# Optimization experiments

Measured on AMD Instinct MI355X. Metric: run time of the kernel, lower is better.

## Reference

```python
import jax, jax.numpy as jnp
import numpy as np

MARGIN = 0.5

def setup_inputs() -> dict:
    key = jax.random.key(0)
    k1, k2 = jax.random.split(key)
    inputs = jax.random.normal(k1, (8192, 256), dtype=jnp.float32)
    target = jax.random.randint(k2, (8192,), 0, 100, dtype=jnp.int64)
    return {"inputs": inputs, "target": target}

def reference(inputs, target):
    N = inputs.shape[0]
    # pairwise squared distances via ||xi||^2 + ||xj||^2 - 2 xi.xj
    sq = jnp.sum(inputs * inputs, axis=1)  # [N]
    gram = inputs @ inputs.T               # [N, N]
    distance = sq[:, None] + sq[None, :] - 2.0 * gram  # [N, N]
    R = (target[None, :] == target[:, None]).astype(inputs.dtype)  # [N, N]
    loss = R * distance + (1.0 - R) * jnp.maximum(MARGIN - distance, 0.0)
    return jnp.sum(loss) / (N * (N - 1.0) * 2.0)
```

## Files before the change

kernel.cpp:

```cpp
#include <hip/hip_runtime.h>
#include <stdint.h>

#define N      8192
#define KDIM   256
#define BM     128
#define TILES  (N / BM)
#define NPAIRS (TILES * (TILES + 1) / 2)
#define MARGIN 0.5f
#define SCALE1 0x7f7f7f7f

typedef float f32x4 __attribute__((ext_vector_type(4)));
typedef int   i32x4 __attribute__((ext_vector_type(4)));
typedef int   i32x8 __attribute__((ext_vector_type(8)));

__device__ __forceinline__ void async_copy16(const void* g, void* l) {
    __builtin_amdgcn_global_load_lds(
        (__attribute__((address_space(1))) void*)(g),
        (__attribute__((address_space(3))) void*)(l),
        16, 0, 0);
}

#if !__has_builtin(__builtin_amdgcn_cvt_pk_fp8_f32)
__device__ __forceinline__ uint32_t f2e4m3(float f) {
    uint32_t u = __float_as_uint(f);
    uint32_t s = (u >> 24) & 0x80u;
    uint32_t au = u & 0x7fffffffu;
    if (au == 0) return s;
    int32_t  exp = (int32_t)(au >> 23) - 127;
    uint32_t man = (au & 0x7fffffu) | 0x800000u;
    uint32_t code;
    if (exp >= -6) {
        code = (uint32_t)((exp + 7) << 3) | ((man >> 20) & 7u);
        uint32_t rem = man & 0xFFFFFu;
        if (rem > 0x80000u || (rem == 0x80000u && (code & 1u))) code++;
    } else {
        int shift = 14 - exp;
        if (shift > 24) return s;
        code = man >> shift;
        uint32_t rem = man & ((1u << shift) - 1u);
        uint32_t h = 1u << (shift - 1);
        if (rem > h || (rem == h && (code & 1u))) code++;
    }
    return s | code;
}
__device__ __forceinline__ uint32_t pack_fp8x4(float4 v) {
    return f2e4m3(v.x) | (f2e4m3(v.y) << 8) | (f2e4m3(v.z) << 16) |
           (f2e4m3(v.w) << 24);
}
#else
__device__ __forceinline__ uint32_t pack_fp8x4(float4 v) {
    int pk = __builtin_amdgcn_cvt_pk_fp8_f32(v.x, v.y, 0, false);
    pk = __builtin_amdgcn_cvt_pk_fp8_f32(v.z, v.w, pk, true);
    return (uint32_t)pk;
}
#endif

__global__ __launch_bounds__(256) void prep_kernel(
        const float* __restrict__ X, uint8_t* __restrict__ Xq,
        float* __restrict__ sq) {
    int row  = blockIdx.x * 4 + (threadIdx.x >> 6);
    int lane = threadIdx.x & 63;

    float4 v = *((const float4*)(X + (size_t)row * KDIM) + lane);
    float ss = v.x * v.x + v.y * v.y + v.z * v.z + v.w * v.w;
    uint32_t pk = pack_fp8x4(v);

    int h   = lane >> 5;
    int g   = (lane >> 2) & 7;
    int pos = g ^ (row & 7);
    *(uint32_t*)(Xq + (size_t)row * 256 + h * 128 + pos * 16 + (lane & 3) * 4) = pk;

    #pragma unroll
    for (int o = 32; o > 0; o >>= 1) ss += __shfl_down(ss, o, 64);
    if (lane == 0) sq[row] = ss;
}

__global__ __launch_bounds__(256, 4) void loss_kernel(
        const uint8_t* __restrict__ Xq, const float* __restrict__ sq,
        const int* __restrict__ tgt, float* __restrict__ partials) {
    const int p = blockIdx.x;
    float tf = 2.0f * TILES + 1.0f;
    int bi = (int)((tf - sqrtf(tf * tf - 8.0f * (float)p)) * 0.5f);
    if (bi < 0) bi = 0;
    while (bi > 0 && (bi * TILES - bi * (bi - 1) / 2) > p) --bi;
    while (((bi + 1) * TILES - (bi + 1) * bi / 2) <= p) ++bi;
    const int bj = bi + (p - (bi * TILES - bi * (bi - 1) / 2));

    __shared__ __align__(16) uint8_t As[BM * 128];
    __shared__ __align__(16) uint8_t Bs[BM * 128];
    __shared__ float sqa_s[BM], sqb_s[BM];
    __shared__ int   ta_s[BM],  tb_s[BM];
    __shared__ float wsum[4];

    const int tid  = threadIdx.x;
    const int wave = tid >> 6;
    const int lane = tid & 63;

    if (tid < 128) {
        sqa_s[tid] = sq[bi * BM + tid];
        ta_s[tid]  = tgt[bi * BM + tid];
    } else {
        int r = tid - 128;
        sqb_s[r] = sq[bj * BM + r];
        tb_s[r]  = tgt[bj * BM + r];
    }

    const int lrow = lane >> 3;
    const int lb   = (lane & 7) * 16;
    const uint8_t* gA = Xq + ((size_t)bi * BM + wave * 32 + lrow) * 256 + lb;
    const uint8_t* gB = Xq + ((size_t)bj * BM + wave * 32 + lrow) * 256 + lb;
    uint8_t* lA = As + wave * 32 * 128;
    uint8_t* lB = Bs + wave * 32 * 128;

    const int frow  = lane & 15;
    const int fquad = lane >> 4;
    const int wm = (wave >> 1) * 64;
    const int wn = (wave & 1) * 64;
    const int key  = frow & 7;
    const int off0 = ((fquad * 2 + 0) ^ key) * 16;
    const int off1 = ((fquad * 2 + 1) ^ key) * 16;
    const uint8_t* aBp = As + (wm + frow) * 128;
    const uint8_t* bBp = Bs + (wn + frow) * 128;

    f32x4 acc[4][4];
    #pragma unroll
    for (int im = 0; im < 4; ++im)
        #pragma unroll
        for (int in = 0; in < 4; ++in)
            acc[im][in] = (f32x4){0.f, 0.f, 0.f, 0.f};

    #pragma unroll
    for (int h = 0; h < 2; ++h) {
        #pragma unroll
        for (int q = 0; q < 4; ++q) {
            async_copy16(gA + h * 128 + q * 8 * 256, lA + q * 1024);
            async_copy16(gB + h * 128 + q * 8 * 256, lB + q * 1024);
        }
        __syncthreads();

        i32x8 a8[4];
        #pragma unroll
        for (int im = 0; im < 4; ++im) {
            i32x4 al = *(const i32x4*)(aBp + im * 16 * 128 + off0);
            i32x4 ah = *(const i32x4*)(aBp + im * 16 * 128 + off1);
            a8[im] = __builtin_shufflevector(al, ah, 0, 1, 2, 3, 4, 5, 6, 7);
        }
        #pragma unroll
        for (int in = 0; in < 4; ++in) {
            i32x4 bl = *(const i32x4*)(bBp + in * 16 * 128 + off0);
            i32x4 bh = *(const i32x4*)(bBp + in * 16 * 128 + off1);
            i32x8 b8 = __builtin_shufflevector(bl, bh, 0, 1, 2, 3, 4, 5, 6, 7);
            #pragma unroll
            for (int im = 0; im < 4; ++im)
                acc[im][in] = __builtin_amdgcn_mfma_scale_f32_16x16x128_f8f6f4(
                    a8[im], b8, acc[im][in], 0, 0,
                    0, SCALE1, 0, SCALE1);
        }
        if (h == 0) __syncthreads();
    }

    float lsum = 0.0f;
    if (bi != bj) {
        #pragma unroll
        for (int im = 0; im < 4; ++im) {
            #pragma unroll
            for (int in = 0; in < 4; ++in) {
                #pragma unroll
                for (int r = 0; r < 4; ++r) {
                    int rl = wm + im * 16 + fquad * 4 + r;
                    int cl = wn + in * 16 + frow;
                    float d = fmaf(-2.0f, acc[im][in][r],
                                   sqa_s[rl] + sqb_s[cl]);
                    lsum += (ta_s[rl] == tb_s[cl]) ? d
                                                   : fmaxf(MARGIN - d, 0.0f);
                }
            }
        }
        lsum *= 2.0f;
    } else {
        #pragma unroll
        for (int im = 0; im < 4; ++im) {
            #pragma unroll
            for (int in = 0; in < 4; ++in) {
                #pragma unroll
                for (int r = 0; r < 4; ++r) {
                    int rl = wm + im * 16 + fquad * 4 + r;
                    int cl = wn + in * 16 + frow;
                    float d = fmaf(-2.0f, acc[im][in][r],
                                   sqa_s[rl] + sqb_s[cl]);
                    float c = (ta_s[rl] == tb_s[cl]) ? d
                                                     : fmaxf(MARGIN - d, 0.0f);
                    float w = (rl < cl) ? 2.0f : ((rl == cl) ? 1.0f : 0.0f);
                    lsum += w * c;
                }
            }
        }
    }

    #pragma unroll
    for (int o = 32; o > 0; o >>= 1) lsum += __shfl_down(lsum, o, 64);
    if (lane == 0) wsum[wave] = lsum;
    __syncthreads();
    if (tid == 0) partials[p] = wsum[0] + wsum[1] + wsum[2] + wsum[3];
}

__global__ __launch_bounds__(256) void reduce_kernel(
        const float* __restrict__ partials, float* __restrict__ out,
        int n, float scale) {
    float s = 0.0f;
    for (int i = threadIdx.x; i < n; i += 256) s += partials[i];
    __shared__ float w[4];
    #pragma unroll
    for (int o = 32; o > 0; o >>= 1) s += __shfl_down(s, o, 64);
    int wave = threadIdx.x >> 6, lane = threadIdx.x & 63;
    if (lane == 0) w[wave] = s;
    __syncthreads();
    if (threadIdx.x == 0) out[0] = (w[0] + w[1] + w[2] + w[3]) * scale;
}

extern "C" void kernel_launch(void* const* d_in, const int* in_sizes, int n_in,
                              void* d_out, int out_size, void* d_ws, size_t ws_size,
                              hipStream_t stream) {
    (void)in_sizes; (void)n_in; (void)out_size; (void)ws_size;
    const float* X   = (const float*)d_in[0];
    const int*   tgt = (const int*)d_in[1];

    uint8_t* Xq     = (uint8_t*)d_ws;
    float* sq       = (float*)((char*)d_ws + (size_t)N * KDIM);
    float* partials = sq + N;

    prep_kernel<<<N / 4, 256, 0, stream>>>(X, Xq, sq);
    loss_kernel<<<NPAIRS, 256, 0, stream>>>(Xq, sq, tgt, partials);

    const float scale = (float)(1.0 / ((double)N * ((double)N - 1.0) * 2.0));
    reduce_kernel<<<1, 256, 0, stream>>>(partials, (float*)d_out, NPAIRS, scale);
}
```

Measured before the change: 81.51 us.

## Make loss kernel persistent with prefetch of next tile pair during epilogue

Replaces the one-block-per-tile-pair launch (2080 blocks) with a fixed grid of 1024 blocks that loop over pairs in strides. The next pair's first K-half and its norms and targets are fetched while the current pair's second half is computed and its epilogue runs, using double-buffered metadata in shared memory. Epilogue metadata now comes from vectorized shared loads. This hides global load latency and cuts launch and tail overhead, at the cost of extra barriers and uneven work, since some blocks handle three pairs and others two.

New measurement: 155.8 us. 1.91x slower.

```diff
diff --git a/kernel.cpp b/kernel.cpp
--- a/kernel.cpp
+++ b/kernel.cpp
@@ -6,6 +6,7 @@
 #define BM     128
 #define TILES  (N / BM)
 #define NPAIRS (TILES * (TILES + 1) / 2)
+#define GRID   1024
 #define MARGIN 0.5f
 #define SCALE1 0x7f7f7f7f
 
@@ -78,130 +79,189 @@
 __global__ __launch_bounds__(256, 4) void loss_kernel(
         const uint8_t* __restrict__ Xq, const float* __restrict__ sq,
         const int* __restrict__ tgt, float* __restrict__ partials) {
-    const int p = blockIdx.x;
-    float tf = 2.0f * TILES + 1.0f;
-    int bi = (int)((tf - sqrtf(tf * tf - 8.0f * (float)p)) * 0.5f);
-    if (bi < 0) bi = 0;
-    while (bi > 0 && (bi * TILES - bi * (bi - 1) / 2) > p) --bi;
-    while (((bi + 1) * TILES - (bi + 1) * bi / 2) <= p) ++bi;
-    const int bj = bi + (p - (bi * TILES - bi * (bi - 1) / 2));
-
     __shared__ __align__(16) uint8_t As[BM * 128];
     __shared__ __align__(16) uint8_t Bs[BM * 128];
-    __shared__ float sqa_s[BM], sqb_s[BM];
-    __shared__ int   ta_s[BM],  tb_s[BM];
+    __shared__ __align__(16) float sqm[2][2][BM];
+    __shared__ __align__(16) int   tm [2][2][BM];
     __shared__ float wsum[4];
 
     const int tid  = threadIdx.x;
     const int wave = tid >> 6;
     const int lane = tid & 63;
 
-    if (tid < 128) {
-        sqa_s[tid] = sq[bi * BM + tid];
-        ta_s[tid]  = tgt[bi * BM + tid];
-    } else {
-        int r = tid - 128;
-        sqb_s[r] = sq[bj * BM + r];
-        tb_s[r]  = tgt[bj * BM + r];
-    }
-
-    const int lrow = lane >> 3;
-    const int lb   = (lane & 7) * 16;
-    const uint8_t* gA = Xq + ((size_t)bi * BM + wave * 32 + lrow) * 256 + lb;
-    const uint8_t* gB = Xq + ((size_t)bj * BM + wave * 32 + lrow) * 256 + lb;
-    uint8_t* lA = As + wave * 32 * 128;
-    uint8_t* lB = Bs + wave * 32 * 128;
-
     const int frow  = lane & 15;
     const int fquad = lane >> 4;
-    const int wm = (wave >> 1) * 64;
-    const int wn = (wave & 1) * 64;
-    const int key  = frow & 7;
+    const int wm  = (wave >> 1) * 64;
+    const int wn  = (wave & 1) * 64;
+    const int key = frow & 7;
     const int off0 = ((fquad * 2 + 0) ^ key) * 16;
     const int off1 = ((fquad * 2 + 1) ^ key) * 16;
     const uint8_t* aBp = As + (wm + frow) * 128;
     const uint8_t* bBp = Bs + (wn + frow) * 128;
 
-    f32x4 acc[4][4];
-    #pragma unroll
-    for (int im = 0; im < 4; ++im)
-        #pragma unroll
-        for (int in = 0; in < 4; ++in)
-            acc[im][in] = (f32x4){0.f, 0.f, 0.f, 0.f};
-
-    #pragma unroll
-    for (int h = 0; h < 2; ++h) {
+    const int lrow = lane >> 3;
+    const int lb   = (lane & 7) * 16;
+    uint8_t* lA = As + wave * 32 * 128;
+    uint8_t* lB = Bs + wave * 32 * 128;
+
+    auto decode = [&](int p, int& bi, int& bj) {
+        float tf = 2.0f * TILES + 1.0f;
+        int b = (int)((tf - sqrtf(tf * tf - 8.0f * (float)p)) * 0.5f);
+        if (b < 0) b = 0;
+        while (b > 0 && (b * TILES - b * (b - 1) / 2) > p) --b;
+        while (((b + 1) * TILES - (b + 1) * b / 2) <= p) ++b;
+        bi = b;
+        bj = b + (p - (b * TILES - b * (b - 1) / 2));
+    };
+    auto stage = [&](int bi, int bj, int h) {
+        const uint8_t* gA =
+            Xq + ((size_t)bi * BM + wave * 32 + lrow) * 256 + lb + h * 128;
+        const uint8_t* gB =
+            Xq + ((size_t)bj * BM + wave * 32 + lrow) * 256 + lb + h * 128;
         #pragma unroll
         for (int q = 0; q < 4; ++q) {
-            async_copy16(gA + h * 128 + q * 8 * 256, lA + q * 1024);
-            async_copy16(gB + h * 128 + q * 8 * 256, lB + q * 1024);
-        }
-        __syncthreads();
-
-        i32x8 a8[4];
+            async_copy16(gA + q * 8 * 256, lA + q * 1024);
+            async_copy16(gB + q * 8 * 256, lB + q * 1024);
+        }
+    };
+    auto meta_fetch = [&](int bi, int bj, float& mv, int& ti) {
+        int r = tid & 127;
+        int base = ((tid < 128) ? bi : bj) * BM + r;
+        mv = sq[base];
+        ti = tgt[base];
+    };
+    auto meta_store = [&](int buf, float mv, int ti) {
+        int r = tid & 127;
+        int ab = (tid < 128) ? 0 : 1;
+        sqm[buf][ab][r] = mv;
+        tm [buf][ab][r] = ti;
+    };
+
+    int p = blockIdx.x;
+    int bi, bj;
+    decode(p, bi, bj);
+    {
+        float mv; int ti;
+        meta_fetch(bi, bj, mv, ti);
+        stage(bi, bj, 0);
+        meta_store(0, mv, ti);
+    }
+    __syncthreads();
+
+    int   buf   = 0;
+    float total = 0.0f;
+
+    while (true) {
+        f32x4 acc[4][4];
+        #pragma unroll
+        for (int im = 0; im < 4; ++im)
+            #pragma unroll
+            for (int in = 0; in < 4; ++in)
+                acc[im][in] = (f32x4){0.f, 0.f, 0.f, 0.f};
+
+        #define COMPUTE()                                                      \
+            do {                                                               \
+                i32x8 a8[4];                                                   \
+                _Pragma("unroll")                                              \
+                for (int im = 0; im < 4; ++im) {                               \
+                    i32x4 al = *(const i32x4*)(aBp + im * 16 * 128 + off0);    \
+                    i32x4 ah = *(const i32x4*)(aBp + im * 16 * 128 + off1);    \
+                    a8[im] = __builtin_shufflevector(al, ah,                   \
+                                                     0, 1, 2, 3, 4, 5, 6, 7); \
+                }                                                              \
+                _Pragma("unroll")                                              \
+                for (int in = 0; in < 4; ++in) {                               \
+                    i32x4 bl = *(const i32x4*)(bBp + in * 16 * 128 + off0);    \
+                    i32x4 bh = *(const i32x4*)(bBp + in * 16 * 128 + off1);    \
+                    i32x8 b8 = __builtin_shufflevector(bl, bh,                 \
+                                                       0, 1, 2, 3, 4, 5, 6, 7);\
+                    _Pragma("unroll")                                          \
+                    for (int im = 0; im < 4; ++im)                             \
+                        acc[im][in] =                                          \
+                            __builtin_amdgcn_mfma_scale_f32_16x16x128_f8f6f4(  \
+                                a8[im], b8, acc[im][in], 0, 0,                 \
+                                0, SCALE1, 0, SCALE1);                         \
+                }                                                              \
+            } while (0)
+
+        COMPUTE();
+        __syncthreads();
+        stage(bi, bj, 1);
+
+        int  pn   = p + GRID;
+        bool more = (pn < NPAIRS);
+        int  bi2 = bi, bj2 = bj;
+        float mv = 0.0f; int ti = 0;
+        if (more) {
+            decode(pn, bi2, bj2);
+            meta_fetch(bi2, bj2, mv, ti);
+        }
+        __syncthreads();
+        COMPUTE();
+        __syncthreads();
+        #undef COMPUTE
+
+        f32x4 sqa4[4]; i32x4 ta4[4];
+        float sqb_l[4]; int tb_l[4];
         #pragma unroll
         for (int im = 0; im < 4; ++im) {
-            i32x4 al = *(const i32x4*)(aBp + im * 16 * 128 + off0);
-            i32x4 ah = *(const i32x4*)(aBp + im * 16 * 128 + off1);
-            a8[im] = __builtin_shufflevector(al, ah, 0, 1, 2, 3, 4, 5, 6, 7);
+            sqa4[im] = *(const f32x4*)&sqm[buf][0][wm + im * 16 + fquad * 4];
+            ta4[im]  = *(const i32x4*)&tm [buf][0][wm + im * 16 + fquad * 4];
         }
         #pragma unroll
         for (int in = 0; in < 4; ++in) {
-            i32x4 bl = *(const i32x4*)(bBp + in * 16 * 128 + off0);
-            i32x4 bh = *(const i32x4*)(bBp + in * 16 * 128 + off1);
-            i32x8 b8 = __builtin_shufflevector(bl, bh, 0, 1, 2, 3, 4, 5, 6, 7);
+            sqb_l[in] = sqm[buf][1][wn + in * 16 + frow];
+            tb_l[in]  = tm [buf][1][wn + in * 16 + frow];
+        }
+
+        if (more) {
+            meta_store(buf ^ 1, mv, ti);
+            stage(bi2, bj2, 0);
+        }
+
+        float ls = 0.0f;
+        if (bi != bj) {
             #pragma unroll
             for (int im = 0; im < 4; ++im)
-                acc[im][in] = __builtin_amdgcn_mfma_scale_f32_16x16x128_f8f6f4(
-                    a8[im], b8, acc[im][in], 0, 0,
-                    0, SCALE1, 0, SCALE1);
-        }
-        if (h == 0) __syncthreads();
+                #pragma unroll
+                for (int in = 0; in < 4; ++in)
+                    #pragma unroll
+                    for (int r = 0; r < 4; ++r) {
+                        float d = fmaf(-2.0f, acc[im][in][r],
+                                       sqa4[im][r] + sqb_l[in]);
+                        ls += (ta4[im][r] == tb_l[in])
+                                  ? d : fmaxf(MARGIN - d, 0.0f);
+                    }
+            total += 2.0f * ls;
+        } else {
+            #pragma unroll
+            for (int im = 0; im < 4; ++im)
+                #pragma unroll
+                for (int in = 0; in < 4; ++in)
+                    #pragma unroll
+                    for (int r = 0; r < 4; ++r) {
+                        int rl = wm + im * 16 + fquad * 4 + r;
+                        int cl = wn + in * 16 + frow;
+                        float d = fmaf(-2.0f, acc[im][in][r],
+                                       sqa4[im][r] + sqb_l[in]);
+                        float c = (ta4[im][r] == tb_l[in])
+                                      ? d : fmaxf(MARGIN - d, 0.0f);
+                        float w = (rl < cl) ? 2.0f : ((rl == cl) ? 1.0f : 0.0f);
+                        ls += w * c;
+                    }
+            total += ls;
+        }
+
+        if (!more) break;
+        p = pn; bi = bi2; bj = bj2; buf ^= 1;
+        __syncthreads();
     }
 
-    float lsum = 0.0f;
-    if (bi != bj) {
-        #pragma unroll
-        for (int im = 0; im < 4; ++im) {
-            #pragma unroll
-            for (int in = 0; in < 4; ++in) {
-                #pragma unroll
-                for (int r = 0; r < 4; ++r) {
-                    int rl = wm + im * 16 + fquad * 4 + r;
-                    int cl = wn + in * 16 + frow;
-                    float d = fmaf(-2.0f, acc[im][in][r],
-                                   sqa_s[rl] + sqb_s[cl]);
-                    lsum += (ta_s[rl] == tb_s[cl]) ? d
-                                                   : fmaxf(MARGIN - d, 0.0f);
-                }
-            }
-        }
-        lsum *= 2.0f;
-    } else {
-        #pragma unroll
-        for (int im = 0; im < 4; ++im) {
-            #pragma unroll
-            for (int in = 0; in < 4; ++in) {
-                #pragma unroll
-                for (int r = 0; r < 4; ++r) {
-                    int rl = wm + im * 16 + fquad * 4 + r;
-                    int cl = wn + in * 16 + frow;
-                    float d = fmaf(-2.0f, acc[im][in][r],
-                                   sqa_s[rl] + sqb_s[cl]);
-                    float c = (ta_s[rl] == tb_s[cl]) ? d
-                                                     : fmaxf(MARGIN - d, 0.0f);
-                    float w = (rl < cl) ? 2.0f : ((rl == cl) ? 1.0f : 0.0f);
-                    lsum += w * c;
-                }
-            }
-        }
-    }
-
     #pragma unroll
-    for (int o = 32; o > 0; o >>= 1) lsum += __shfl_down(lsum, o, 64);
-    if (lane == 0) wsum[wave] = lsum;
+    for (int o = 32; o > 0; o >>= 1) total += __shfl_down(total, o, 64);
+    if (lane == 0) wsum[wave] = total;
     __syncthreads();
-    if (tid == 0) partials[p] = wsum[0] + wsum[1] + wsum[2] + wsum[3];
+    if (tid == 0) partials[blockIdx.x] = wsum[0] + wsum[1] + wsum[2] + wsum[3];
 }
 
 __global__ __launch_bounds__(256) void reduce_kernel(
@@ -230,8 +290,8 @@
     float* partials = sq + N;
 
     prep_kernel<<<N / 4, 256, 0, stream>>>(X, Xq, sq);
-    loss_kernel<<<NPAIRS, 256, 0, stream>>>(Xq, sq, tgt, partials);
+    loss_kernel<<<GRID, 256, 0, stream>>>(Xq, sq, tgt, partials);
 
     const float scale = (float)(1.0 / ((double)N * ((double)N - 1.0) * 2.0));
-    reduce_kernel<<<1, 256, 0, stream>>>(partials, (float*)d_out, NPAIRS, scale);
-}
+    reduce_kernel<<<1, 256, 0, stream>>>(partials, (float*)d_out, GRID, scale);
+}
```
